# Kernel optimization log

Measured on AMD Instinct MI355X. Metric: run time of the kernel, lower is better.

## Reference

```python
import jax, jax.numpy as jnp
import numpy as np

N, E, F = 50000, 1_600_000, 128
EPS = 1e-5
DATASET_NUM = 1.0


def _glorot(k, shape):
    lim = jnp.sqrt(6.0 / (shape[0] + shape[1]))
    return jax.random.uniform(k, shape, jnp.float32, -lim, lim)


def setup_inputs() -> dict:
    key = jax.random.key(0)
    ks = jax.random.split(key, 24)
    inp = {
        "x": jax.random.normal(ks[0], (N, F), jnp.float32),
        "noise": jax.random.normal(ks[1], (N, F), jnp.float32),
        "edge_index": jax.random.randint(ks[2], (2, E), 0, N, jnp.int64),
        # ChebConv K=2 weights: W0 (T_0 = x term), W1 (T_1 = L_hat x term)
        "W1_0": _glorot(ks[3], (F, 64)),  "W1_1": _glorot(ks[4], (F, 64)),  "b1": jnp.zeros((64,), jnp.float32),
        "g1": jnp.ones((64,), jnp.float32), "be1": jnp.zeros((64,), jnp.float32),
        "W2_0": _glorot(ks[5], (64, 16)), "W2_1": _glorot(ks[6], (64, 16)), "b2": jnp.zeros((16,), jnp.float32),
        "W3_0": _glorot(ks[7], (16, 64)), "W3_1": _glorot(ks[8], (16, 64)), "b3": jnp.zeros((64,), jnp.float32),
        "g3": jnp.ones((64,), jnp.float32), "be3": jnp.zeros((64,), jnp.float32),
        "W4_0": _glorot(ks[9], (64, F)),  "W4_1": _glorot(ks[10], (64, F)), "b4": jnp.zeros((F,), jnp.float32),
    }
    return inp


def reference(x, noise, edge_index, W1_0, W1_1, b1, g1, be1,
              W2_0, W2_1, b2, W3_0, W3_1, b3, g3, be3, W4_0, W4_1, b4):
    src, dst = edge_index[0], edge_index[1]
    n = x.shape[0]

    # train-mode noise injection: x + dataset_num * randn * x.mean()
    x = x + DATASET_NUM * noise * jnp.mean(x)

    # symmetric normalization; with lambda_max=2 the scaled Laplacian is -A_norm
    deg = jax.ops.segment_sum(jnp.ones_like(src, dtype=x.dtype), dst, num_segments=n)
    dinv = jnp.where(deg > 0, jax.lax.rsqrt(jnp.maximum(deg, 1.0)), 0.0)
    w_e = dinv[src] * dinv[dst]  # [E]

    def cheb(h, W0, W1, b):
        # T_0 = h ; T_1 = L_hat h = -A_norm h  (K=2 ChebConv)
        tx1 = -jax.ops.segment_sum(w_e[:, None] * h[src], dst, num_segments=n)
        return h @ W0 + tx1 @ W1 + b

    def bn(h, g, be):
        mu = jnp.mean(h, axis=0)
        var = jnp.mean((h - mu) ** 2, axis=0)
        return g * (h - mu) * jax.lax.rsqrt(var + EPS) + be

    h1 = jax.nn.relu(bn(cheb(x, W1_0, W1_1, b1), g1, be1))
    h2 = cheb(h1, W2_0, W2_1, b2)
    h3 = jax.nn.relu(bn(cheb(h2, W3_0, W3_1, b3), g3, be3))
    return cheb(h3, W4_0, W4_1, b4)
```

## Files before the change

### kernel.cpp

```cpp
#include <hip/hip_runtime.h>

#define NNODES 50000
#define NEDGES 1600000
#define FEAT   128
#define EPSV   1e-5f

__device__ __forceinline__ float4 f4fma(float w, float4 r, float4 a) {
  a.x = fmaf(w, r.x, a.x); a.y = fmaf(w, r.y, a.y);
  a.z = fmaf(w, r.z, a.z); a.w = fmaf(w, r.w, a.w);
  return a;
}
__device__ __forceinline__ float4 f4bnrelu(float4 r, float4 s, float4 t) {
  float4 o;
  o.x = fmaxf(fmaf(r.x, s.x, t.x), 0.f);
  o.y = fmaxf(fmaf(r.y, s.y, t.y), 0.f);
  o.z = fmaxf(fmaf(r.z, s.z, t.z), 0.f);
  o.w = fmaxf(fmaf(r.w, s.w, t.w), 0.f);
  return o;
}

__global__ __launch_bounds__(256) void sum_kernel(const float* __restrict__ x,
                                                  float* __restrict__ out, int n4) {
  const float4* x4 = (const float4*)x;
  float s = 0.f;
  for (int i = blockIdx.x * blockDim.x + threadIdx.x; i < n4; i += gridDim.x * blockDim.x) {
    float4 v = x4[i];
    s += v.x + v.y + v.z + v.w;
  }
  for (int off = 32; off > 0; off >>= 1) s += __shfl_down(s, off);
  __shared__ float ls[4];
  int wid = threadIdx.x >> 6;
  if ((threadIdx.x & 63) == 0) ls[wid] = s;
  __syncthreads();
  if (threadIdx.x == 0) atomicAdd(out, ls[0] + ls[1] + ls[2] + ls[3]);
}

__global__ __launch_bounds__(256) void degree_kernel(const int* __restrict__ ei,
                                                     int* __restrict__ degi, int ne) {
  int e = blockIdx.x * blockDim.x + threadIdx.x;
  if (e < ne) atomicAdd(&degi[ei[NEDGES + e]], 1);
}

__global__ __launch_bounds__(256) void dinv_kernel(const int* __restrict__ degi,
                                                   float* __restrict__ dinv, int n) {
  int i = blockIdx.x * blockDim.x + threadIdx.x;
  if (i < n) dinv[i] = (degi[i] > 0) ? rsqrtf((float)degi[i]) : 0.f;
}

__global__ __launch_bounds__(1024) void scan1_kernel(const int* __restrict__ cnt,
                                                     int* __restrict__ exc,
                                                     int* __restrict__ bsum, int n) {
  __shared__ int s[1024];
  int tid = threadIdx.x;
  int i = blockIdx.x * 1024 + tid;
  int v = (i < n) ? cnt[i] : 0;
  int val = v;
  s[tid] = v;
  __syncthreads();
  for (int off = 1; off < 1024; off <<= 1) {
    int t = (tid >= off) ? s[tid - off] : 0;
    __syncthreads();
    val += t;
    s[tid] = val;
    __syncthreads();
  }
  if (i < n) exc[i] = val - v;
  if (tid == 1023) bsum[blockIdx.x] = val;
}

__global__ __launch_bounds__(256) void scan2_kernel(int* __restrict__ bsum, int nb) {
  __shared__ int s[256];
  int tid = threadIdx.x;
  int v = (tid < nb) ? bsum[tid] : 0;
  int val = v;
  s[tid] = v;
  __syncthreads();
  for (int off = 1; off < 256; off <<= 1) {
    int t = (tid >= off) ? s[tid - off] : 0;
    __syncthreads();
    val += t;
    s[tid] = val;
    __syncthreads();
  }
  if (tid < nb) bsum[tid] = val - v;
}

__global__ __launch_bounds__(256) void scan3_kernel(int* __restrict__ row_ptr,
                                                    const int* __restrict__ bsum,
                                                    int* __restrict__ cursor, int n) {
  int i = blockIdx.x * blockDim.x + threadIdx.x;
  if (i < n) {
    int v = row_ptr[i] + bsum[i >> 10];
    row_ptr[i] = v;
    cursor[i] = v;
  } else if (i == n) {
    row_ptr[n] = NEDGES;
  }
}

__global__ __launch_bounds__(256) void csr_fill_kernel(const int* __restrict__ ei,
                                                       const float* __restrict__ dinv,
                                                       int* __restrict__ cursor,
                                                       int2* __restrict__ ep, int ne) {
  int e = blockIdx.x * blockDim.x + threadIdx.x;
  if (e >= ne) return;
  int s = ei[e];
  int d = ei[NEDGES + e];
  float w = dinv[s] * dinv[d];
  int pos = atomicAdd(&cursor[d], 1);
  ep[pos] = make_int2(s, __float_as_int(w));
}

template <int F, int S, int OFF, bool ADD, bool STATS, bool BNIN>
__global__ __launch_bounds__(256) void spmm_kernel(
    const int* __restrict__ row_ptr, const int2* __restrict__ ep,
    const float* __restrict__ mat, const float* __restrict__ bias,
    const float* __restrict__ stats_in, const float* __restrict__ gin,
    const float* __restrict__ bein, float* __restrict__ stats_out,
    float* __restrict__ out, int n) {
  constexpr int LPN = F / 4;
  constexpr int NPB = 256 / LPN;
  __shared__ float sst[STATS ? 2 * F : 1];
  if (STATS) {
    if (threadIdx.x < 2 * F) sst[threadIdx.x] = 0.f;
    __syncthreads();
  }
  const int lane = threadIdx.x & (LPN - 1);
  const int g = threadIdx.x / LPN;
  const int node = blockIdx.x * NPB + g;
  const int f0 = lane * 4;
  float4 scl = make_float4(0.f, 0.f, 0.f, 0.f), sht = scl;
  if (BNIN) {
    const float inv_n = 1.0f / (float)n;
    float4 su = *(const float4*)&stats_in[f0];
    float4 sq = *(const float4*)&stats_in[F + f0];
    float4 gg = *(const float4*)&gin[f0];
    float4 bb = *(const float4*)&bein[f0];
    float mu;
    mu = su.x * inv_n; scl.x = gg.x * rsqrtf(sq.x * inv_n - mu * mu + EPSV); sht.x = bb.x - mu * scl.x;
    mu = su.y * inv_n; scl.y = gg.y * rsqrtf(sq.y * inv_n - mu * mu + EPSV); sht.y = bb.y - mu * scl.y;
    mu = su.z * inv_n; scl.z = gg.z * rsqrtf(sq.z * inv_n - mu * mu + EPSV); sht.z = bb.z - mu * scl.z;
    mu = su.w * inv_n; scl.w = gg.w * rsqrtf(sq.w * inv_n - mu * mu + EPSV); sht.w = bb.w - mu * scl.w;
  }
  if (node < n) {
    const float* mb = mat + OFF + f0;
    int e = row_ptr[node];
    const int end = row_ptr[node + 1];
    float4 a0 = make_float4(0.f, 0.f, 0.f, 0.f), a1 = a0, a2 = a0, a3 = a0;
    for (; e + 3 < end; e += 4) {
      int2 s0 = ep[e], s1 = ep[e + 1], s2 = ep[e + 2], s3 = ep[e + 3];
      float4 r0 = *(const float4*)(mb + (size_t)s0.x * S);
      float4 r1 = *(const float4*)(mb + (size_t)s1.x * S);
      float4 r2 = *(const float4*)(mb + (size_t)s2.x * S);
      float4 r3 = *(const float4*)(mb + (size_t)s3.x * S);
      if (BNIN) {
        r0 = f4bnrelu(r0, scl, sht); r1 = f4bnrelu(r1, scl, sht);
        r2 = f4bnrelu(r2, scl, sht); r3 = f4bnrelu(r3, scl, sht);
      }
      a0 = f4fma(__int_as_float(s0.y), r0, a0);
      a1 = f4fma(__int_as_float(s1.y), r1, a1);
      a2 = f4fma(__int_as_float(s2.y), r2, a2);
      a3 = f4fma(__int_as_float(s3.y), r3, a3);
    }
    for (; e < end; ++e) {
      int2 s0 = ep[e];
      float4 r0 = *(const float4*)(mb + (size_t)s0.x * S);
      if (BNIN) r0 = f4bnrelu(r0, scl, sht);
      a0 = f4fma(__int_as_float(s0.y), r0, a0);
    }
    float4 o;
    o.x = (a0.x + a1.x) + (a2.x + a3.x);
    o.y = (a0.y + a1.y) + (a2.y + a3.y);
    o.z = (a0.z + a1.z) + (a2.z + a3.z);
    o.w = (a0.w + a1.w) + (a2.w + a3.w);
    if (ADD) {
      float4 base = *(const float4*)&mat[(size_t)node * S + f0];
      float4 b4 = *(const float4*)&bias[f0];
      o.x = base.x + b4.x - o.x; o.y = base.y + b4.y - o.y;
      o.z = base.z + b4.z - o.z; o.w = base.w + b4.w - o.w;
    } else {
      o.x = -o.x; o.y = -o.y; o.z = -o.z; o.w = -o.w;
    }
    *(float4*)&out[(size_t)node * F + f0] = o;
    if (STATS) {
      atomicAdd(&sst[f0 + 0], o.x); atomicAdd(&sst[F + f0 + 0], o.x * o.x);
      atomicAdd(&sst[f0 + 1], o.y); atomicAdd(&sst[F + f0 + 1], o.y * o.y);
      atomicAdd(&sst[f0 + 2], o.z); atomicAdd(&sst[F + f0 + 2], o.z * o.z);
      atomicAdd(&sst[f0 + 3], o.w); atomicAdd(&sst[F + f0 + 3], o.w * o.w);
    }
  }
  if (STATS) {
    __syncthreads();
    if (threadIdx.x < 2 * F) atomicAdd(&stats_out[threadIdx.x], sst[threadIdx.x]);
  }
}

template <int K, int NB, int NT, bool ROWCAT, bool BIAS, bool BNIN, bool STATS, bool NOISE>
__global__ __launch_bounds__(256) void gemm_kernel(
    const float* __restrict__ A1, const float* __restrict__ A2,
    const float* __restrict__ W0, const float* __restrict__ W1,
    const float* __restrict__ bias, int col0,
    const float* __restrict__ noise, const float* __restrict__ sumv,
    const float* __restrict__ stats_in, const float* __restrict__ gin,
    const float* __restrict__ bein, float* __restrict__ stats_out,
    float* __restrict__ out, int n) {
  constexpr int TC  = NB / 4;
  constexpr int RG  = 256 / TC;
  constexpr int RPT = 4;
  constexpr int RPB = RG * RPT;
  constexpr int AP  = (K == 128) ? K : (K + 1);
  constexpr int KB  = ROWCAT ? K / 2 : K;
  __shared__ float wl[K * NB];
  __shared__ float al[RPB * AP];
  __shared__ float sarr[BNIN ? KB : 1];
  __shared__ float tarr[BNIN ? KB : 1];
  __shared__ float sst[STATS ? 2 * NB : 1];
  const int tid = threadIdx.x;
  if (STATS && tid < 2 * NB) sst[tid] = 0.f;
  if (BNIN) {
    const float inv_n = 1.0f / (float)n;
    for (int f = tid; f < KB; f += 256) {
      float mu = stats_in[f] * inv_n;
      float var = stats_in[KB + f] * inv_n - mu * mu;
      float s = gin[f] * rsqrtf(var + EPSV);
      sarr[f] = s;
      tarr[f] = bein[f] - mu * s;
    }
    __syncthreads();
  }
  float mean = 0.f;
  if (NOISE) mean = sumv[0] * (1.0f / (float)(NNODES * FEAT));

  for (int i = tid; i < K * NB; i += 256) {
    int k = i / NB, j = i - k * NB;
    int jg = col0 + j;
    float v;
    if (ROWCAT) v = (k < K / 2) ? W0[k * NT + jg] : W1[(k - K / 2) * NT + jg];
    else        v = (jg < NT / 2) ? W0[k * (NT / 2) + jg] : W1[k * (NT / 2) + (jg - NT / 2)];
    wl[i] = v;
  }
  const int row0 = blockIdx.x * RPB;
  for (int i = tid; i < RPB * K; i += 256) {
    int r = i / K, k = i - r * K;
    int gr = row0 + r;
    float v = 0.f;
    if (gr < n) {
      if (ROWCAT) {
        if (k < K / 2) {
          v = A1[(size_t)gr * (K / 2) + k];
          if (BNIN) v = fmaxf(fmaf(v, sarr[k], tarr[k]), 0.f);
        } else {
          v = A2[(size_t)gr * (K / 2) + (k - K / 2)];
        }
      } else {
        v = A1[(size_t)gr * K + k];
        if (BNIN) v = fmaxf(fmaf(v, sarr[k], tarr[k]), 0.f);
        if (NOISE) v = fmaf(noise[(size_t)gr * K + k], mean, v);
      }
    }
    al[r * AP + k] = v;
  }
  __syncthreads();

  const int jt = (tid % TC) * 4;
  const int rbase = (tid / TC) * RPT;
  float acc[RPT][4] = {};
#pragma unroll 4
  for (int k = 0; k < K; ++k) {
    float4 w4 = *(const float4*)&wl[k * NB + jt];
#pragma unroll
    for (int rr = 0; rr < RPT; ++rr) {
      float a = al[(rbase + rr) * AP + k];
      acc[rr][0] = fmaf(a, w4.x, acc[rr][0]);
      acc[rr][1] = fmaf(a, w4.y, acc[rr][1]);
      acc[rr][2] = fmaf(a, w4.z, acc[rr][2]);
      acc[rr][3] = fmaf(a, w4.w, acc[rr][3]);
    }
  }
  float4 b4 = make_float4(0.f, 0.f, 0.f, 0.f);
  if (BIAS) b4 = *(const float4*)&bias[col0 + jt];
  float sl[4] = {}, ql[4] = {};
#pragma unroll
  for (int rr = 0; rr < RPT; ++rr) {
    int gr = row0 + rbase + rr;
    if (gr < n) {
      float o0 = acc[rr][0] + b4.x, o1 = acc[rr][1] + b4.y;
      float o2 = acc[rr][2] + b4.z, o3 = acc[rr][3] + b4.w;
      float4 o = make_float4(o0, o1, o2, o3);
      *(float4*)&out[(size_t)gr * NT + col0 + jt] = o;
      if (STATS) {
        sl[0] += o0; ql[0] += o0 * o0; sl[1] += o1; ql[1] += o1 * o1;
        sl[2] += o2; ql[2] += o2 * o2; sl[3] += o3; ql[3] += o3 * o3;
      }
    }
  }
  if (STATS) {
#pragma unroll
    for (int j = 0; j < 4; ++j) {
      atomicAdd(&sst[jt + j], sl[j]);
      atomicAdd(&sst[NB + jt + j], ql[j]);
    }
    __syncthreads();
    if (tid < 2 * NB) atomicAdd(&stats_out[tid], sst[tid]);
  }
}

extern "C" void kernel_launch(void* const* d_in, const int* in_sizes, int n_in,
                              void* d_out, int out_size, void* d_ws, size_t ws_size,
                              hipStream_t stream) {
  const float* x     = (const float*)d_in[0];
  const float* noise = (const float*)d_in[1];
  const int*   ei    = (const int*)d_in[2];
  const float* W1_0 = (const float*)d_in[3];
  const float* W1_1 = (const float*)d_in[4];
  const float* b1   = (const float*)d_in[5];
  const float* g1   = (const float*)d_in[6];
  const float* be1  = (const float*)d_in[7];
  const float* W2_0 = (const float*)d_in[8];
  const float* W2_1 = (const float*)d_in[9];
  const float* b2   = (const float*)d_in[10];
  const float* W3_0 = (const float*)d_in[11];
  const float* W3_1 = (const float*)d_in[12];
  const float* b3   = (const float*)d_in[13];
  const float* g3   = (const float*)d_in[14];
  const float* be3  = (const float*)d_in[15];
  const float* W4_0 = (const float*)d_in[16];
  const float* W4_1 = (const float*)d_in[17];
  const float* b4   = (const float*)d_in[18];
  float* out = (float*)d_out;

  char* p = (char*)d_ws;
  size_t off = 0;
  auto alloc = [&](size_t b) -> void* {
    void* r = p + off;
    off += (b + 255) & ~(size_t)255;
    return r;
  };
  float* s_sum  = (float*)alloc(4);
  float* stats0 = (float*)alloc(2 * 64 * 4);
  float* stats1 = (float*)alloc(2 * 64 * 4);
  int*   degi   = (int*)alloc(sizeof(int) * NNODES);
  size_t zero_bytes = off;
  float* dinv    = (float*)alloc(sizeof(float) * NNODES);
  int*   row_ptr = (int*)alloc(sizeof(int) * (NNODES + 1));
  int*   bsum    = (int*)alloc(256 * sizeof(int));
  int*   cursor  = (int*)alloc(sizeof(int) * NNODES);
  int2*  ep      = (int2*)alloc(8ULL * NEDGES);
  float* big1    = (float*)alloc(4ULL * NNODES * FEAT);
  float* h1      = (float*)alloc(4ULL * NNODES * 64);

  float* big0 = out;
  float* zz2  = big0;
  float* h2   = big0 + (size_t)NNODES * 32;
  float* agg3 = big0 + (size_t)NNODES * 48;
  float* zz1  = big1;
  float* h3   = big1;
  float* agg4 = big1 + (size_t)NNODES * 64;

  hipMemsetAsync(d_ws, 0, zero_bytes, stream);

  int n4 = NNODES * FEAT / 4;
  sum_kernel<<<2048, 256, 0, stream>>>(x, s_sum, n4);
  degree_kernel<<<(NEDGES + 255) / 256, 256, 0, stream>>>(ei, degi, NEDGES);
  dinv_kernel<<<(NNODES + 255) / 256, 256, 0, stream>>>(degi, dinv, NNODES);
  scan1_kernel<<<(NNODES + 1023) / 1024, 1024, 0, stream>>>(degi, row_ptr, bsum, NNODES);
  scan2_kernel<<<1, 256, 0, stream>>>(bsum, (NNODES + 1023) / 1024);
  scan3_kernel<<<(NNODES + 256) / 256, 256, 0, stream>>>(row_ptr, bsum, cursor, NNODES);
  csr_fill_kernel<<<(NEDGES + 255) / 256, 256, 0, stream>>>(ei, dinv, cursor, ep, NEDGES);

  gemm_kernel<128, 64, 128, false, false, false, false, true>
      <<<(NNODES + 63) / 64, 256, 0, stream>>>(x, nullptr, W1_0, W1_1, nullptr, 0,
          noise, s_sum, nullptr, nullptr, nullptr, nullptr, zz1, NNODES);
  gemm_kernel<128, 64, 128, false, false, false, false, true>
      <<<(NNODES + 63) / 64, 256, 0, stream>>>(x, nullptr, W1_0, W1_1, nullptr, 64,
          noise, s_sum, nullptr, nullptr, nullptr, nullptr, zz1, NNODES);
  spmm_kernel<64, 128, 64, true, true, false><<<(NNODES + 15) / 16, 256, 0, stream>>>(
      row_ptr, ep, zz1, b1, nullptr, nullptr, nullptr, stats0, h1, NNODES);

  gemm_kernel<64, 32, 32, false, false, true, false, false>
      <<<(NNODES + 127) / 128, 256, 0, stream>>>(h1, nullptr, W2_0, W2_1, nullptr, 0,
          nullptr, nullptr, stats0, g1, be1, nullptr, zz2, NNODES);
  spmm_kernel<16, 32, 16, true, false, false><<<(NNODES + 63) / 64, 256, 0, stream>>>(
      row_ptr, ep, zz2, b2, nullptr, nullptr, nullptr, nullptr, h2, NNODES);

  spmm_kernel<16, 16, 0, false, false, false><<<(NNODES + 63) / 64, 256, 0, stream>>>(
      row_ptr, ep, h2, nullptr, nullptr, nullptr, nullptr, nullptr, agg3, NNODES);
  gemm_kernel<32, 64, 64, true, true, false, true, false>
      <<<(NNODES + 63) / 64, 256, 0, stream>>>(h2, agg3, W3_0, W3_1, b3, 0,
          nullptr, nullptr, nullptr, nullptr, nullptr, stats1, h3, NNODES);

  spmm_kernel<64, 64, 0, false, false, true><<<(NNODES + 15) / 16, 256, 0, stream>>>(
      row_ptr, ep, h3, nullptr, stats1, g3, be3, nullptr, agg4, NNODES);
  gemm_kernel<128, 64, 128, true, true, true, false, false>
      <<<(NNODES + 63) / 64, 256, 0, stream>>>(h3, agg4, W4_0, W4_1, b4, 0,
          nullptr, nullptr, stats1, g3, be3, nullptr, out, NNODES);
  gemm_kernel<128, 64, 128, true, true, true, false, false>
      <<<(NNODES + 63) / 64, 256, 0, stream>>>(h3, agg4, W4_0, W4_1, b4, 64,
          nullptr, nullptr, stats1, g3, be3, nullptr, out, NNODES);
}
```

Baseline: 736.8 us.

## Gather fp16 features in SpMM with wave-per-node edge-parallel aggregation

The features gathered by the sparse aggregation (the right half of the layer-1 and layer-2 projections, h2, h3) are now stored in fp16, which halves the bytes per random gather. The SpMM is restructured so each wavefront handles one node, with lanes split across edges and 8-wide half vectors, followed by a shuffle reduction over a grid-stride loop. The GEMM also gains a float4-vectorised k loop, padded shared-memory rows, and output modes that write fp16 or split fp32/fp16 buffers. This trades accuracy, since fp16 storage rounds the features, for less gather bandwidth and better load balance on high-degree rows.

```diff
diff --git a/kernel.cpp b/kernel.cpp
--- a/kernel.cpp
+++ b/kernel.cpp
@@ -5,18 +5,13 @@
 #define FEAT   128
 #define EPSV   1e-5f
 
-__device__ __forceinline__ float4 f4fma(float w, float4 r, float4 a) {
-  a.x = fmaf(w, r.x, a.x); a.y = fmaf(w, r.y, a.y);
-  a.z = fmaf(w, r.z, a.z); a.w = fmaf(w, r.w, a.w);
+typedef _Float16 h8 __attribute__((ext_vector_type(8)));
+typedef _Float16 h4 __attribute__((ext_vector_type(4)));
+
+__device__ __forceinline__ float4 f4fma(float s, float4 w, float4 a) {
+  a.x = fmaf(s, w.x, a.x); a.y = fmaf(s, w.y, a.y);
+  a.z = fmaf(s, w.z, a.z); a.w = fmaf(s, w.w, a.w);
   return a;
-}
-__device__ __forceinline__ float4 f4bnrelu(float4 r, float4 s, float4 t) {
-  float4 o;
-  o.x = fmaxf(fmaf(r.x, s.x, t.x), 0.f);
-  o.y = fmaxf(fmaf(r.y, s.y, t.y), 0.f);
-  o.z = fmaxf(fmaf(r.z, s.z, t.z), 0.f);
-  o.w = fmaxf(fmaf(r.w, s.w, t.w), 0.f);
-  return o;
 }
 
 __global__ __launch_bounds__(256) void sum_kernel(const float* __restrict__ x,
@@ -111,104 +106,125 @@
   ep[pos] = make_int2(s, __float_as_int(w));
 }
 
-template <int F, int S, int OFF, bool ADD, bool STATS, bool BNIN>
+template <int F, bool ADD, bool STATS, bool BNIN, bool OUTH>
 __global__ __launch_bounds__(256) void spmm_kernel(
     const int* __restrict__ row_ptr, const int2* __restrict__ ep,
-    const float* __restrict__ mat, const float* __restrict__ bias,
+    const _Float16* __restrict__ gsrc, const float* __restrict__ addL,
+    const float* __restrict__ bias,
     const float* __restrict__ stats_in, const float* __restrict__ gin,
     const float* __restrict__ bein, float* __restrict__ stats_out,
-    float* __restrict__ out, int n) {
-  constexpr int LPN = F / 4;
-  constexpr int NPB = 256 / LPN;
+    void* __restrict__ outv, int n) {
+  constexpr int LPE = F / 8;
+  constexpr int EPC = 64 / LPE;
+  constexpr int LG  = (LPE == 2) ? 1 : 3;
   __shared__ float sst[STATS ? 2 * F : 1];
+  const int tid = threadIdx.x;
   if (STATS) {
-    if (threadIdx.x < 2 * F) sst[threadIdx.x] = 0.f;
-    __syncthreads();
-  }
-  const int lane = threadIdx.x & (LPN - 1);
-  const int g = threadIdx.x / LPN;
-  const int node = blockIdx.x * NPB + g;
-  const int f0 = lane * 4;
-  float4 scl = make_float4(0.f, 0.f, 0.f, 0.f), sht = scl;
+    if (tid < 2 * F) sst[tid] = 0.f;
+    __syncthreads();
+  }
+  const int lane = tid & 63;
+  const int wv = tid >> 6;
+  const int sub = lane & (LPE - 1);
+  const int g = lane >> LG;
+  const int f0 = sub * 8;
+  float scl[8], sht[8];
   if (BNIN) {
     const float inv_n = 1.0f / (float)n;
-    float4 su = *(const float4*)&stats_in[f0];
-    float4 sq = *(const float4*)&stats_in[F + f0];
-    float4 gg = *(const float4*)&gin[f0];
-    float4 bb = *(const float4*)&bein[f0];
-    float mu;
-    mu = su.x * inv_n; scl.x = gg.x * rsqrtf(sq.x * inv_n - mu * mu + EPSV); sht.x = bb.x - mu * scl.x;
-    mu = su.y * inv_n; scl.y = gg.y * rsqrtf(sq.y * inv_n - mu * mu + EPSV); sht.y = bb.y - mu * scl.y;
-    mu = su.z * inv_n; scl.z = gg.z * rsqrtf(sq.z * inv_n - mu * mu + EPSV); sht.z = bb.z - mu * scl.z;
-    mu = su.w * inv_n; scl.w = gg.w * rsqrtf(sq.w * inv_n - mu * mu + EPSV); sht.w = bb.w - mu * scl.w;
-  }
-  if (node < n) {
-    const float* mb = mat + OFF + f0;
-    int e = row_ptr[node];
-    const int end = row_ptr[node + 1];
-    float4 a0 = make_float4(0.f, 0.f, 0.f, 0.f), a1 = a0, a2 = a0, a3 = a0;
-    for (; e + 3 < end; e += 4) {
-      int2 s0 = ep[e], s1 = ep[e + 1], s2 = ep[e + 2], s3 = ep[e + 3];
-      float4 r0 = *(const float4*)(mb + (size_t)s0.x * S);
-      float4 r1 = *(const float4*)(mb + (size_t)s1.x * S);
-      float4 r2 = *(const float4*)(mb + (size_t)s2.x * S);
-      float4 r3 = *(const float4*)(mb + (size_t)s3.x * S);
-      if (BNIN) {
-        r0 = f4bnrelu(r0, scl, sht); r1 = f4bnrelu(r1, scl, sht);
-        r2 = f4bnrelu(r2, scl, sht); r3 = f4bnrelu(r3, scl, sht);
-      }
-      a0 = f4fma(__int_as_float(s0.y), r0, a0);
-      a1 = f4fma(__int_as_float(s1.y), r1, a1);
-      a2 = f4fma(__int_as_float(s2.y), r2, a2);
-      a3 = f4fma(__int_as_float(s3.y), r3, a3);
-    }
-    for (; e < end; ++e) {
+#pragma unroll
+    for (int j = 0; j < 8; ++j) {
+      int f = f0 + j;
+      float mu = stats_in[f] * inv_n;
+      float var = stats_in[F + f] * inv_n - mu * mu;
+      float s = gin[f] * rsqrtf(var + EPSV);
+      scl[j] = s;
+      sht[j] = bein[f] - mu * s;
+    }
+  }
+  for (int node = blockIdx.x * 4 + wv; node < n; node += gridDim.x * 4) {
+    float acc[8] = {};
+    const int beg = row_ptr[node], end = row_ptr[node + 1];
+    int e = beg + g;
+    while (e < end) {
       int2 s0 = ep[e];
-      float4 r0 = *(const float4*)(mb + (size_t)s0.x * S);
-      if (BNIN) r0 = f4bnrelu(r0, scl, sht);
-      a0 = f4fma(__int_as_float(s0.y), r0, a0);
-    }
-    float4 o;
-    o.x = (a0.x + a1.x) + (a2.x + a3.x);
-    o.y = (a0.y + a1.y) + (a2.y + a3.y);
-    o.z = (a0.z + a1.z) + (a2.z + a3.z);
-    o.w = (a0.w + a1.w) + (a2.w + a3.w);
-    if (ADD) {
-      float4 base = *(const float4*)&mat[(size_t)node * S + f0];
-      float4 b4 = *(const float4*)&bias[f0];
-      o.x = base.x + b4.x - o.x; o.y = base.y + b4.y - o.y;
-      o.z = base.z + b4.z - o.z; o.w = base.w + b4.w - o.w;
-    } else {
-      o.x = -o.x; o.y = -o.y; o.z = -o.z; o.w = -o.w;
-    }
-    *(float4*)&out[(size_t)node * F + f0] = o;
-    if (STATS) {
-      atomicAdd(&sst[f0 + 0], o.x); atomicAdd(&sst[F + f0 + 0], o.x * o.x);
-      atomicAdd(&sst[f0 + 1], o.y); atomicAdd(&sst[F + f0 + 1], o.y * o.y);
-      atomicAdd(&sst[f0 + 2], o.z); atomicAdd(&sst[F + f0 + 2], o.z * o.z);
-      atomicAdd(&sst[f0 + 3], o.w); atomicAdd(&sst[F + f0 + 3], o.w * o.w);
+      bool p1 = (e + EPC) < end;
+      int2 s1 = ep[p1 ? e + EPC : e];
+      float w0 = __int_as_float(s0.y);
+      float w1 = p1 ? __int_as_float(s1.y) : 0.f;
+      h8 r0 = *(const h8*)(gsrc + (size_t)s0.x * F + f0);
+      h8 r1 = *(const h8*)(gsrc + (size_t)s1.x * F + f0);
+#pragma unroll
+      for (int j = 0; j < 8; ++j) {
+        float v0 = (float)r0[j], v1 = (float)r1[j];
+        if (BNIN) {
+          v0 = fmaxf(fmaf(v0, scl[j], sht[j]), 0.f);
+          v1 = fmaxf(fmaf(v1, scl[j], sht[j]), 0.f);
+        }
+        acc[j] = fmaf(w0, v0, acc[j]);
+        acc[j] = fmaf(w1, v1, acc[j]);
+      }
+      e += 2 * EPC;
+    }
+#pragma unroll
+    for (int m = LPE; m < 64; m <<= 1) {
+#pragma unroll
+      for (int j = 0; j < 8; ++j) acc[j] += __shfl_xor(acc[j], m);
+    }
+    if (lane < LPE) {
+      float o[8];
+      if (ADD) {
+        float4 a0 = *(const float4*)&addL[(size_t)node * F + f0];
+        float4 a1 = *(const float4*)&addL[(size_t)node * F + f0 + 4];
+        float4 b0 = *(const float4*)&bias[f0];
+        float4 b1 = *(const float4*)&bias[f0 + 4];
+        o[0] = a0.x + b0.x - acc[0]; o[1] = a0.y + b0.y - acc[1];
+        o[2] = a0.z + b0.z - acc[2]; o[3] = a0.w + b0.w - acc[3];
+        o[4] = a1.x + b1.x - acc[4]; o[5] = a1.y + b1.y - acc[5];
+        o[6] = a1.z + b1.z - acc[6]; o[7] = a1.w + b1.w - acc[7];
+      } else {
+#pragma unroll
+        for (int j = 0; j < 8; ++j) o[j] = -acc[j];
+      }
+      if (OUTH) {
+        h8 ho;
+#pragma unroll
+        for (int j = 0; j < 8; ++j) ho[j] = (_Float16)o[j];
+        *(h8*)((_Float16*)outv + (size_t)node * F + f0) = ho;
+      } else {
+        float* op = (float*)outv + (size_t)node * F + f0;
+        *(float4*)op = make_float4(o[0], o[1], o[2], o[3]);
+        *(float4*)(op + 4) = make_float4(o[4], o[5], o[6], o[7]);
+      }
+      if (STATS) {
+#pragma unroll
+        for (int j = 0; j < 8; ++j) {
+          atomicAdd(&sst[f0 + j], o[j]);
+          atomicAdd(&sst[F + f0 + j], o[j] * o[j]);
+        }
+      }
     }
   }
   if (STATS) {
     __syncthreads();
-    if (threadIdx.x < 2 * F) atomicAdd(&stats_out[threadIdx.x], sst[threadIdx.x]);
-  }
-}
-
-template <int K, int NB, int NT, bool ROWCAT, bool BIAS, bool BNIN, bool STATS, bool NOISE>
+    if (tid < 2 * F) atomicAdd(&stats_out[tid], sst[tid]);
+  }
+}
+
+template <int K, int NB, bool ROWCAT, bool BIAS, bool BNIN, bool STATS, bool NOISE,
+          bool A1H, int OMODE>
 __global__ __launch_bounds__(256) void gemm_kernel(
-    const float* __restrict__ A1, const float* __restrict__ A2,
+    const void* __restrict__ A1, const float* __restrict__ A2,
     const float* __restrict__ W0, const float* __restrict__ W1,
-    const float* __restrict__ bias, int col0,
+    const float* __restrict__ bias, int col0, int wnt, int ostride, int ocol0,
     const float* __restrict__ noise, const float* __restrict__ sumv,
     const float* __restrict__ stats_in, const float* __restrict__ gin,
     const float* __restrict__ bein, float* __restrict__ stats_out,
-    float* __restrict__ out, int n) {
+    void* __restrict__ outv, void* __restrict__ out2, int n) {
   constexpr int TC  = NB / 4;
   constexpr int RG  = 256 / TC;
   constexpr int RPT = 4;
   constexpr int RPB = RG * RPT;
-  constexpr int AP  = (K == 128) ? K : (K + 1);
+  constexpr int AP  = K + 4;
   constexpr int KB  = ROWCAT ? K / 2 : K;
   __shared__ float wl[K * NB];
   __shared__ float al[RPB * AP];
@@ -226,7 +242,6 @@
       sarr[f] = s;
       tarr[f] = bein[f] - mu * s;
     }
-    __syncthreads();
   }
   float mean = 0.f;
   if (NOISE) mean = sumv[0] * (1.0f / (float)(NNODES * FEAT));
@@ -235,10 +250,12 @@
     int k = i / NB, j = i - k * NB;
     int jg = col0 + j;
     float v;
-    if (ROWCAT) v = (k < K / 2) ? W0[k * NT + jg] : W1[(k - K / 2) * NT + jg];
-    else        v = (jg < NT / 2) ? W0[k * (NT / 2) + jg] : W1[k * (NT / 2) + (jg - NT / 2)];
+    if (ROWCAT) v = (k < K / 2) ? W0[k * wnt + jg] : W1[(k - K / 2) * wnt + jg];
+    else        v = (jg < wnt / 2) ? W0[k * (wnt / 2) + jg] : W1[k * (wnt / 2) + (jg - wnt / 2)];
     wl[i] = v;
   }
+  __syncthreads();
+
   const int row0 = blockIdx.x * RPB;
   for (int i = tid; i < RPB * K; i += 256) {
     int r = i / K, k = i - r * K;
@@ -247,13 +264,15 @@
     if (gr < n) {
       if (ROWCAT) {
         if (k < K / 2) {
-          v = A1[(size_t)gr * (K / 2) + k];
+          v = A1H ? (float)((const _Float16*)A1)[(size_t)gr * (K / 2) + k]
+                  : ((const float*)A1)[(size_t)gr * (K / 2) + k];
           if (BNIN) v = fmaxf(fmaf(v, sarr[k], tarr[k]), 0.f);
         } else {
           v = A2[(size_t)gr * (K / 2) + (k - K / 2)];
         }
       } else {
-        v = A1[(size_t)gr * K + k];
+        v = A1H ? (float)((const _Float16*)A1)[(size_t)gr * K + k]
+                : ((const float*)A1)[(size_t)gr * K + k];
         if (BNIN) v = fmaxf(fmaf(v, sarr[k], tarr[k]), 0.f);
         if (NOISE) v = fmaf(noise[(size_t)gr * K + k], mean, v);
       }
@@ -264,17 +283,24 @@
 
   const int jt = (tid % TC) * 4;
   const int rbase = (tid / TC) * RPT;
-  float acc[RPT][4] = {};
+  float4 acc[RPT];
+#pragma unroll
+  for (int rr = 0; rr < RPT; ++rr) acc[rr] = make_float4(0.f, 0.f, 0.f, 0.f);
+  const float4* wl4 = (const float4*)wl;
+  const int jt4 = jt >> 2;
 #pragma unroll 4
-  for (int k = 0; k < K; ++k) {
-    float4 w4 = *(const float4*)&wl[k * NB + jt];
+  for (int k0 = 0; k0 < K; k0 += 4) {
+    float4 w0 = wl4[(k0 + 0) * TC + jt4];
+    float4 w1 = wl4[(k0 + 1) * TC + jt4];
+    float4 w2 = wl4[(k0 + 2) * TC + jt4];
+    float4 w3 = wl4[(k0 + 3) * TC + jt4];
 #pragma unroll
     for (int rr = 0; rr < RPT; ++rr) {
-      float a = al[(rbase + rr) * AP + k];
-      acc[rr][0] = fmaf(a, w4.x, acc[rr][0]);
-      acc[rr][1] = fmaf(a, w4.y, acc[rr][1]);
-      acc[rr][2] = fmaf(a, w4.z, acc[rr][2]);
-      acc[rr][3] = fmaf(a, w4.w, acc[rr][3]);
+      float4 a = *(const float4*)&al[(rbase + rr) * AP + k0];
+      acc[rr] = f4fma(a.x, w0, acc[rr]);
+      acc[rr] = f4fma(a.y, w1, acc[rr]);
+      acc[rr] = f4fma(a.z, w2, acc[rr]);
+      acc[rr] = f4fma(a.w, w3, acc[rr]);
     }
   }
   float4 b4 = make_float4(0.f, 0.f, 0.f, 0.f);
@@ -284,13 +310,27 @@
   for (int rr = 0; rr < RPT; ++rr) {
     int gr = row0 + rbase + rr;
     if (gr < n) {
-      float o0 = acc[rr][0] + b4.x, o1 = acc[rr][1] + b4.y;
-      float o2 = acc[rr][2] + b4.z, o3 = acc[rr][3] + b4.w;
-      float4 o = make_float4(o0, o1, o2, o3);
-      *(float4*)&out[(size_t)gr * NT + col0 + jt] = o;
+      float4 o;
+      o.x = acc[rr].x + b4.x; o.y = acc[rr].y + b4.y;
+      o.z = acc[rr].z + b4.z; o.w = acc[rr].w + b4.w;
+      if (OMODE == 0) {
+        *(float4*)((float*)outv + (size_t)gr * ostride + ocol0 + jt) = o;
+      } else if (OMODE == 1) {
+        h4 ho; ho[0] = (_Float16)o.x; ho[1] = (_Float16)o.y;
+        ho[2] = (_Float16)o.z; ho[3] = (_Float16)o.w;
+        *(h4*)((_Float16*)outv + (size_t)gr * ostride + ocol0 + jt) = ho;
+      } else {
+        if (jt < 16) {
+          *(float4*)((float*)outv + (size_t)gr * 16 + jt) = o;
+        } else {
+          h4 ho; ho[0] = (_Float16)o.x; ho[1] = (_Float16)o.y;
+          ho[2] = (_Float16)o.z; ho[3] = (_Float16)o.w;
+          *(h4*)((_Float16*)out2 + (size_t)gr * 16 + (jt - 16)) = ho;
+        }
+      }
       if (STATS) {
-        sl[0] += o0; ql[0] += o0 * o0; sl[1] += o1; ql[1] += o1 * o1;
-        sl[2] += o2; ql[2] += o2 * o2; sl[3] += o3; ql[3] += o3 * o3;
+        sl[0] += o.x; ql[0] += o.x * o.x; sl[1] += o.y; ql[1] += o.y * o.y;
+        sl[2] += o.z; ql[2] += o.z * o.z; sl[3] += o.w; ql[3] += o.w * o.w;
       }
     }
   }
@@ -341,21 +381,21 @@
   float* stats1 = (float*)alloc(2 * 64 * 4);
   int*   degi   = (int*)alloc(sizeof(int) * NNODES);
   size_t zero_bytes = off;
-  float* dinv    = (float*)alloc(sizeof(float) * NNODES);
-  int*   row_ptr = (int*)alloc(sizeof(int) * (NNODES + 1));
-  int*   bsum    = (int*)alloc(256 * sizeof(int));
-  int*   cursor  = (int*)alloc(sizeof(int) * NNODES);
-  int2*  ep      = (int2*)alloc(8ULL * NEDGES);
-  float* big1    = (float*)alloc(4ULL * NNODES * FEAT);
-  float* h1      = (float*)alloc(4ULL * NNODES * 64);
-
-  float* big0 = out;
-  float* zz2  = big0;
-  float* h2   = big0 + (size_t)NNODES * 32;
-  float* agg3 = big0 + (size_t)NNODES * 48;
-  float* zz1  = big1;
-  float* h3   = big1;
-  float* agg4 = big1 + (size_t)NNODES * 64;
+  float*     dinv    = (float*)alloc(sizeof(float) * NNODES);
+  int*       row_ptr = (int*)alloc(sizeof(int) * (NNODES + 1));
+  int*       bsum    = (int*)alloc(256 * sizeof(int));
+  int*       cursor  = (int*)alloc(sizeof(int) * NNODES);
+  int2*      ep      = (int2*)alloc(8ULL * NEDGES);
+  float*     zzL     = (float*)alloc(4ULL * NNODES * 64);
+  _Float16*  zzRh    = (_Float16*)alloc(2ULL * NNODES * 64);
+  float*     h1      = (float*)alloc(4ULL * NNODES * 64);
+  _Float16*  zz2Rh   = (_Float16*)alloc(2ULL * NNODES * 16);
+  _Float16*  h2      = (_Float16*)alloc(2ULL * NNODES * 16);
+  _Float16*  h3h     = (_Float16*)alloc(2ULL * NNODES * 64);
+  float*     agg4    = zzL;
+
+  float* zz2L = out;
+  float* agg3 = out + (size_t)NNODES * 16;
 
   hipMemsetAsync(d_ws, 0, zero_bytes, stream);
 
@@ -368,33 +408,39 @@
   scan3_kernel<<<(NNODES + 256) / 256, 256, 0, stream>>>(row_ptr, bsum, cursor, NNODES);
   csr_fill_kernel<<<(NEDGES + 255) / 256, 256, 0, stream>>>(ei, dinv, cursor, ep, NEDGES);
 
-  gemm_kernel<128, 64, 128, false, false, false, false, true>
-      <<<(NNODES + 63) / 64, 256, 0, stream>>>(x, nullptr, W1_0, W1_1, nullptr, 0,
-          noise, s_sum, nullptr, nullptr, nullptr, nullptr, zz1, NNODES);
-  gemm_kernel<128, 64, 128, false, false, false, false, true>
-      <<<(NNODES + 63) / 64, 256, 0, stream>>>(x, nullptr, W1_0, W1_1, nullptr, 64,
-          noise, s_sum, nullptr, nullptr, nullptr, nullptr, zz1, NNODES);
-  spmm_kernel<64, 128, 64, true, true, false><<<(NNODES + 15) / 16, 256, 0, stream>>>(
-      row_ptr, ep, zz1, b1, nullptr, nullptr, nullptr, stats0, h1, NNODES);
-
-  gemm_kernel<64, 32, 32, false, false, true, false, false>
-      <<<(NNODES + 127) / 128, 256, 0, stream>>>(h1, nullptr, W2_0, W2_1, nullptr, 0,
-          nullptr, nullptr, stats0, g1, be1, nullptr, zz2, NNODES);
-  spmm_kernel<16, 32, 16, true, false, false><<<(NNODES + 63) / 64, 256, 0, stream>>>(
-      row_ptr, ep, zz2, b2, nullptr, nullptr, nullptr, nullptr, h2, NNODES);
-
-  spmm_kernel<16, 16, 0, false, false, false><<<(NNODES + 63) / 64, 256, 0, stream>>>(
-      row_ptr, ep, h2, nullptr, nullptr, nullptr, nullptr, nullptr, agg3, NNODES);
-  gemm_kernel<32, 64, 64, true, true, false, true, false>
-      <<<(NNODES + 63) / 64, 256, 0, stream>>>(h2, agg3, W3_0, W3_1, b3, 0,
-          nullptr, nullptr, nullptr, nullptr, nullptr, stats1, h3, NNODES);
-
-  spmm_kernel<64, 64, 0, false, false, true><<<(NNODES + 15) / 16, 256, 0, stream>>>(
-      row_ptr, ep, h3, nullptr, stats1, g3, be3, nullptr, agg4, NNODES);
-  gemm_kernel<128, 64, 128, true, true, true, false, false>
-      <<<(NNODES + 63) / 64, 256, 0, stream>>>(h3, agg4, W4_0, W4_1, b4, 0,
-          nullptr, nullptr, stats1, g3, be3, nullptr, out, NNODES);
-  gemm_kernel<128, 64, 128, true, true, true, false, false>
-      <<<(NNODES + 63) / 64, 256, 0, stream>>>(h3, agg4, W4_0, W4_1, b4, 64,
-          nullptr, nullptr, stats1, g3, be3, nullptr, out, NNODES);
-}
+  gemm_kernel<128, 64, false, false, false, false, true, false, 0>
+      <<<(NNODES + 63) / 64, 256, 0, stream>>>(
+      x, nullptr, W1_0, W1_1, nullptr, 0, 128, 64, 0,
+      noise, s_sum, nullptr, nullptr, nullptr, nullptr, zzL, nullptr, NNODES);
+  gemm_kernel<128, 64, false, false, false, false, true, false, 1>
+      <<<(NNODES + 63) / 64, 256, 0, stream>>>(
+      x, nullptr, W1_0, W1_1, nullptr, 64, 128, 64, 0,
+      noise, s_sum, nullptr, nullptr, nullptr, nullptr, zzRh, nullptr, NNODES);
+  spmm_kernel<64, true, true, false, false><<<2048, 256, 0, stream>>>(
+      row_ptr, ep, zzRh, zzL, b1, nullptr, nullptr, nullptr, stats0, h1, NNODES);
+
+  gemm_kernel<64, 32, false, false, true, false, false, false, 2>
+      <<<(NNODES + 127) / 128, 256, 0, stream>>>(
+      h1, nullptr, W2_0, W2_1, nullptr, 0, 32, 16, 0,
+      nullptr, nullptr, stats0, g1, be1, nullptr, zz2L, zz2Rh, NNODES);
+  spmm_kernel<16, true, false, false, true><<<2048, 256, 0, stream>>>(
+      row_ptr, ep, zz2Rh, zz2L, b2, nullptr, nullptr, nullptr, nullptr, h2, NNODES);
+
+  spmm_kernel<16, false, false, false, false><<<2048, 256, 0, stream>>>(
+      row_ptr, ep, h2, nullptr, nullptr, nullptr, nullptr, nullptr, nullptr, agg3, NNODES);
+  gemm_kernel<32, 64, true, true, false, true, false, true, 1>
+      <<<(NNODES + 63) / 64, 256, 0, stream>>>(
+      h2, agg3, W3_0, W3_1, b3, 0, 64, 64, 0,
+      nullptr, nullptr, nullptr, nullptr, nullptr, stats1, h3h, nullptr, NNODES);
+
+  spmm_kernel<64, false, false, true, false><<<2048, 256, 0, stream>>>(
+      row_ptr, ep, h3h, nullptr, nullptr, stats1, g3, be3, nullptr, agg4, NNODES);
+  gemm_kernel<128, 64, true, true, true, false, false, true, 0>
+      <<<(NNODES + 63) / 64, 256, 0, stream>>>(
+      h3h, agg4, W4_0, W4_1, b4, 0, 128, 128, 0,
+      nullptr, nullptr, stats1, g3, be3, nullptr, out, nullptr, NNODES);
+  gemm_kernel<128, 64, true, true, true, false, false, true, 0>
+      <<<(NNODES + 63) / 64, 256, 0, stream>>>(
+      h3h, agg4, W4_0, W4_1, b4, 64, 128, 128, 64,
+      nullptr, nullptr, stats1, g3, be3, nullptr, out, nullptr, NNODES);
+}
```

Result: faster. 683.5 us (-7.2%).
